# Kernel optimization log

Hardware: AMD Instinct MI355X
Metric: run time of the kernel (lower is better)

Reference implementation:

```python
import jax, jax.numpy as jnp
import numpy as np

EPS = 1e-6
NUM_HEADS = 16

def _rmsnorm(h, w):
    hf = h.astype(jnp.float32)
    var = jnp.mean(hf * hf, axis=-1, keepdims=True)
    return (w * (hf * jax.lax.rsqrt(var + EPS))).astype(h.dtype)

def _rotary(t, cos, sin):
    # t: [B,N,H,hd]; cos/sin: [N, hd//2]
    tf = t.astype(jnp.float32)
    tr = tf[..., 0::2]
    ti = tf[..., 1::2]
    c = cos[None, :, None, :]
    s = sin[None, :, None, :]
    out_r = tr * c - ti * s
    out_i = tr * s + ti * c
    out = jnp.stack([out_r, out_i], axis=-1).reshape(t.shape)
    return out.astype(t.dtype)

def setup_inputs() -> dict:
    key = jax.random.key(0)
    ks = jax.random.split(key, 8)
    B, N, C = 2, 2048, 1024
    hd = C // NUM_HEADS
    x = jax.random.normal(ks[0], (B, N, C), jnp.float32)
    qkv_w = jax.random.normal(ks[1], (3 * C, C), jnp.float32) * (C ** -0.5)
    q_norm_w = jnp.ones((hd,), jnp.float32)
    k_norm_w = jnp.ones((hd,), jnp.float32)
    proj_w = jax.random.normal(ks[2], (C, C), jnp.float32) * (C ** -0.5)
    proj_b = jnp.zeros((C,), jnp.float32)
    # rotary freqs_cis = exp(i * theta): unit-magnitude cos/sin
    inv_freq = 1.0 / (10000.0 ** (jnp.arange(0, hd, 2, dtype=jnp.float32) / hd))
    ang = jnp.arange(N, dtype=jnp.float32)[:, None] * inv_freq[None, :]
    pos_cos = jnp.cos(ang)
    pos_sin = jnp.sin(ang)
    mask = jnp.tril(jnp.ones((N, N), dtype=bool))
    return {"x": x, "qkv_w": qkv_w, "q_norm_w": q_norm_w, "k_norm_w": k_norm_w,
            "proj_w": proj_w, "proj_b": proj_b, "pos_cos": pos_cos,
            "pos_sin": pos_sin, "mask": mask}

def reference(x, qkv_w, q_norm_w, k_norm_w, proj_w, proj_b, pos_cos, pos_sin, mask):
    B, N, C = x.shape
    H = NUM_HEADS
    hd = C // H
    qkv = (x @ qkv_w.T).reshape(B, N, 3, H, hd)
    q, k, v = qkv[:, :, 0], qkv[:, :, 1], qkv[:, :, 2]  # [B,N,H,hd]
    q = _rmsnorm(q, q_norm_w)
    k = _rmsnorm(k, k_norm_w)
    q = _rotary(q, pos_cos, pos_sin)
    k = _rotary(k, pos_cos, pos_sin)
    q = q.transpose(0, 2, 1, 3)  # [B,H,N,hd]
    k = k.transpose(0, 2, 1, 3)
    v = v.transpose(0, 2, 1, 3)
    scale = hd ** -0.5
    scores = jnp.einsum('bhqd,bhkd->bhqk', q, k) * scale
    scores = jnp.where(mask[None, None, :, :], scores, jnp.float32(-1e30))
    attn = jax.nn.softmax(scores, axis=-1)
    out = jnp.einsum('bhqk,bhkd->bhqd', attn, v)
    out = out.transpose(0, 2, 1, 3).reshape(B, N, C)
    return out @ proj_w.T + proj_b
```

## Files before the change

### kernel.cpp

```cpp
#include <hip/hip_runtime.h>

using u16 = unsigned short;
using short4v = __attribute__((ext_vector_type(4))) short;
using short8 = __attribute__((ext_vector_type(8))) short;
using floatx4 = __attribute__((ext_vector_type(4))) float;

__device__ __forceinline__ float bf2f(u16 h) {
  union { unsigned int u; float f; } v;
  v.u = ((unsigned int)h) << 16;
  return v.f;
}
__device__ __forceinline__ u16 f2bf(float f) {
  union { float f; unsigned int u; } v;
  v.f = f;
  unsigned int u = v.u;
  return (u16)((u + 0x7FFFu + ((u >> 16) & 1u)) >> 16);
}
__device__ __forceinline__ u16 f2bf_rtz(float f) {
  union { float f; unsigned int u; } v;
  v.f = f;
  return (u16)(v.u >> 16);
}

typedef const __attribute__((address_space(1))) unsigned int* gas_t;
typedef __attribute__((address_space(3))) unsigned int* las_t;
__device__ __forceinline__ void gl_lds16(const u16* g, u16* l) {
  __builtin_amdgcn_global_load_lds((gas_t)(const void*)g, (las_t)(void*)l, 16,
                                   0, 0);
}

#define QSCALE 0.180336880111f

__global__ __launch_bounds__(256) void cvt_all(
    const float* __restrict__ x, const float* __restrict__ wq,
    const float* __restrict__ wp, u16* __restrict__ xb, u16* __restrict__ wqb,
    u16* __restrict__ wpb) {
  int i = blockIdx.x * 256 + threadIdx.x;
  const float* src;
  u16* dst;
  int off;
  if (i < 1048576) {
    src = x; dst = xb; off = i;
  } else if (i < 1048576 + 786432) {
    src = wq; dst = wqb; off = i - 1048576;
  } else {
    src = wp; dst = wpb; off = i - 1835008;
  }
  float4 v = ((const float4*)src)[off];
  ushort4 o;
  o.x = f2bf(v.x);
  o.y = f2bf(v.y);
  o.z = f2bf(v.z);
  o.w = f2bf(v.w);
  ((ushort4*)dst)[off] = o;
}

template <int BIAS, int OUTBF16, int MT>
__global__ __launch_bounds__(256) void gemm_nt(
    const u16* __restrict__ A, const u16* __restrict__ B,
    const float* __restrict__ bias, void* __restrict__ Cout,
    int M, int N, int K) {
  constexpr int ROWS_A = MT * 32;
  __shared__ u16 As[ROWS_A * 32];
  __shared__ u16 Bs[128 * 32];
  const int tid = threadIdx.x;
  const int lane = tid & 63;
  const int wave = tid >> 6;
  const int col = lane & 15;
  const int quad = lane >> 4;
  const int bm = blockIdx.y * ROWS_A;
  const int bn = blockIdx.x * 128;
  const int wm = (wave >> 1) * (MT * 16);
  const int wn = (wave & 1) * 64;

  floatx4 acc[MT][4] = {};

  for (int kb = 0; kb < K; kb += 32) {
    __syncthreads();
#pragma unroll
    for (int c = tid; c < ROWS_A * 4; c += 256)
      gl_lds16(A + (size_t)(bm + (c >> 2)) * K + kb + (c & 3) * 8, As + c * 8);
#pragma unroll
    for (int c = tid; c < 512; c += 256)
      gl_lds16(B + (size_t)(bn + (c >> 2)) * K + kb + (c & 3) * 8, Bs + c * 8);
    __syncthreads();

    short8 af[MT], bfr[4];
#pragma unroll
    for (int i = 0; i < MT; i++)
      af[i] = *(const short8*)(As + (wm + i * 16 + col) * 32 + quad * 8);
#pragma unroll
    for (int i = 0; i < 4; i++)
      bfr[i] = *(const short8*)(Bs + (wn + i * 16 + col) * 32 + quad * 8);
#pragma unroll
    for (int mi = 0; mi < MT; mi++)
#pragma unroll
      for (int ni = 0; ni < 4; ni++)
        acc[mi][ni] = __builtin_amdgcn_mfma_f32_16x16x32_bf16(
            af[mi], bfr[ni], acc[mi][ni], 0, 0, 0);
  }

#pragma unroll
  for (int mi = 0; mi < MT; mi++) {
#pragma unroll
    for (int ni = 0; ni < 4; ni++) {
#pragma unroll
      for (int r = 0; r < 4; r++) {
        int row = bm + wm + mi * 16 + quad * 4 + r;
        int c = bn + wn + ni * 16 + col;
        float v = acc[mi][ni][r];
        if (BIAS) v += bias[c];
        if (OUTBF16)
          ((u16*)Cout)[(size_t)row * N + c] = f2bf(v);
        else
          ((float*)Cout)[(size_t)row * N + c] = v;
      }
    }
  }
}

__global__ __launch_bounds__(256) void rope_v(
    const u16* __restrict__ qkv, const float* __restrict__ qw,
    const float* __restrict__ kw, const float* __restrict__ pcos,
    const float* __restrict__ psin, u16* __restrict__ Qb,
    u16* __restrict__ Kb, u16* __restrict__ Vt) {
  __shared__ u16 T[64 * 68];
  const int bh = blockIdx.x;
  const int n0 = blockIdx.y * 64;
  const int b = bh >> 4, h = bh & 15;
  const int tid = threadIdx.x;
  const int lane = tid & 63;
  const int wave = tid >> 6;

  const float qwl = qw[lane];
  const float kwl = kw[lane];
  for (int tt = 0; tt < 16; tt++) {
    const int n = n0 + wave * 16 + tt;
    const int t = b * 2048 + n;
    const u16* base = qkv + (size_t)t * 3072 + h * 64 + lane;
    float qv = bf2f(base[0]);
    float kv = bf2f(base[1024]);

    float sq = qv * qv, sk = kv * kv;
#pragma unroll
    for (int off = 32; off; off >>= 1) {
      sq += __shfl_xor(sq, off);
      sk += __shfl_xor(sk, off);
    }
    float qn = qv * rsqrtf(sq * (1.0f / 64.0f) + 1e-6f) * qwl;
    float kn = kv * rsqrtf(sk * (1.0f / 64.0f) + 1e-6f) * kwl;

    const int i = lane >> 1;
    const float c = pcos[n * 32 + i];
    const float s = psin[n * 32 + i];
    float qp = __shfl_xor(qn, 1);
    float kp = __shfl_xor(kn, 1);
    float qr, kr;
    if (lane & 1) {
      qr = qp * s + qn * c;
      kr = kp * s + kn * c;
    } else {
      qr = qn * c - qp * s;
      kr = kn * c - kp * s;
    }
    qr *= QSCALE;

    const size_t o = ((size_t)bh * 2048 + n) * 64 + lane;
    Qb[o] = f2bf(qr);
    Kb[o] = f2bf(kr);
  }

  const int q = tid & 7;
  const int r = tid >> 3;
#pragma unroll
  for (int rr = r; rr < 64; rr += 32) {
    short8 v = *(const short8*)(qkv + (size_t)(b * 2048 + n0 + rr) * 3072 +
                                2048 + h * 64 + q * 8);
    *(short8*)&T[rr * 68 + q * 8] = v;
  }
  __syncthreads();
#pragma unroll
  for (int dd = r; dd < 64; dd += 32) {
    short8 o;
#pragma unroll
    for (int j = 0; j < 8; j++) o[j] = T[(q * 8 + j) * 68 + dd];
    *(short8*)(Vt + (size_t)(bh * 64 + dd) * 2048 + n0 + q * 8) = o;
  }
}

#define PSTR 68
__global__ __launch_bounds__(256) void attn_flash(
    const u16* __restrict__ Q, const u16* __restrict__ Kk,
    const u16* __restrict__ Vt, u16* __restrict__ O) {
  __shared__ u16 Ks[2][2][64 * 32];
  __shared__ u16 Vs[2][2][64 * 32];
  __shared__ u16 Pb[4][16 * PSTR];
  const int id = blockIdx.x;
  const int bh = id & 31;
  const int tile = 31 - (id >> 5);
  const int tid = threadIdx.x;
  const int lane = tid & 63;
  const int wave = tid >> 6;
  const int col = lane & 15;
  const int quad = lane >> 4;
  const int srow = tid >> 2;
  const int sswz = ((tid & 3) ^ (srow & 3)) * 8;
  const int rq = (quad ^ (col & 3)) * 8;

  const u16* Qh = Q + (size_t)bh * 2048 * 64;
  const u16* Kh = Kk + (size_t)bh * 2048 * 64;
  const u16* Vh = Vt + (size_t)bh * 64 * 2048;
  const int b = bh >> 4, h = bh & 15;

  const int q0 = tile * 64 + wave * 16;

  short8 aq[2];
#pragma unroll
  for (int ks = 0; ks < 2; ks++)
    aq[ks] = *(const short8*)(Qh + (size_t)(q0 + col) * 64 + ks * 32 + quad * 8);

  short8 ones;
#pragma unroll
  for (int j = 0; j < 8; j++) ones[j] = (short)0x3F80;

  floatx4 accO[4] = {};
  floatx4 lacc = {};
  const int nsteps = tile + 1;

#pragma unroll
  for (int half = 0; half < 2; half++) {
    gl_lds16(Kh + (size_t)srow * 64 + half * 32 + sswz,
             &Ks[0][half][0] + tid * 8);
    gl_lds16(Vh + (size_t)srow * 2048 + half * 32 + sswz,
             &Vs[0][half][0] + tid * 8);
  }
  __syncthreads();

  int cur = 0;
  for (int kt = 0; kt < nsteps; kt++) {
    const int j0 = kt * 64;

    if (kt + 1 < nsteps) {
      const int j1 = j0 + 64;
#pragma unroll
      for (int half = 0; half < 2; half++) {
        gl_lds16(Kh + (size_t)(j1 + srow) * 64 + half * 32 + sswz,
                 &Ks[cur ^ 1][half][0] + tid * 8);
        gl_lds16(Vh + (size_t)srow * 2048 + j1 + half * 32 + sswz,
                 &Vs[cur ^ 1][half][0] + tid * 8);
      }
    }

    floatx4 s[4] = {};
#pragma unroll
    for (int nt = 0; nt < 4; nt++) {
#pragma unroll
      for (int ks = 0; ks < 2; ks++) {
        short8 bk = *(const short8*)&Ks[cur][ks][(nt * 16 + col) * 32 + rq];
        s[nt] =
            __builtin_amdgcn_mfma_f32_16x16x32_bf16(bk, aq[ks], s[nt], 0, 0, 0);
      }
    }

    if (j0 + 63 <= q0) {
#pragma unroll
      for (int nt = 0; nt < 4; nt++) {
        short4v pk;
#pragma unroll
        for (int r = 0; r < 4; r++)
          pk[r] = (short)f2bf_rtz(exp2f(s[nt][r]));
        *(short4v*)&Pb[wave][col * PSTR + nt * 16 + quad * 4] = pk;
      }
    } else {
      const int qg = q0 + col;
#pragma unroll
      for (int nt = 0; nt < 4; nt++) {
        const int jgb = j0 + nt * 16 + quad * 4;
        short4v pk;
#pragma unroll
        for (int r = 0; r < 4; r++) {
          float pv = (jgb + r <= qg) ? exp2f(s[nt][r]) : 0.0f;
          ll_unused:;
          pk[r] = (short)f2bf_rtz(pv);
        }
        *(short4v*)&Pb[wave][col * PSTR + nt * 16 + quad * 4] = pk;
      }
    }

    short8 ap[2];
#pragma unroll
    for (int kf = 0; kf < 2; kf++)
      ap[kf] = *(const short8*)&Pb[wave][col * PSTR + kf * 32 + quad * 8];

#pragma unroll
    for (int kf = 0; kf < 2; kf++)
      lacc = __builtin_amdgcn_mfma_f32_16x16x32_bf16(ap[kf], ones, lacc, 0, 0,
                                                     0);

#pragma unroll
    for (int nt = 0; nt < 4; nt++) {
#pragma unroll
      for (int kf = 0; kf < 2; kf++) {
        short8 bv = *(const short8*)&Vs[cur][kf][(nt * 16 + col) * 32 + rq];
        accO[nt] = __builtin_amdgcn_mfma_f32_16x16x32_bf16(ap[kf], bv,
                                                           accO[nt], 0, 0, 0);
      }
    }

    __syncthreads();
    cur ^= 1;
  }

  float lrec[4];
#pragma unroll
  for (int r = 0; r < 4; r++) lrec[r] = 1.0f / lacc[r];

#pragma unroll
  for (int nt = 0; nt < 4; nt++) {
#pragma unroll
    for (int r = 0; r < 4; r++) {
      int qg = q0 + quad * 4 + r;
      int d = nt * 16 + col;
      O[((size_t)(b * 2048 + qg) * 16 + h) * 64 + d] =
          f2bf(accO[nt][r] * lrec[r]);
    }
  }
}

extern "C" void kernel_launch(void* const* d_in, const int* in_sizes, int n_in,
                              void* d_out, int out_size, void* d_ws,
                              size_t ws_size, hipStream_t stream) {
  const float* x = (const float*)d_in[0];
  const float* qkv_w = (const float*)d_in[1];
  const float* q_norm_w = (const float*)d_in[2];
  const float* k_norm_w = (const float*)d_in[3];
  const float* proj_w = (const float*)d_in[4];
  const float* proj_b = (const float*)d_in[5];
  const float* pos_cos = (const float*)d_in[6];
  const float* pos_sin = (const float*)d_in[7];

  char* ws = (char*)d_ws;
  u16* xb = (u16*)ws;
  u16* wqkvb = (u16*)(ws + 8388608);
  u16* wprojb = (u16*)(ws + 14680064);
  u16* qkv = (u16*)(ws + 16777216);
  u16* Qb = (u16*)(ws + 41943040);
  u16* Kb = (u16*)(ws + 50331648);
  u16* Vt = (u16*)(ws + 58720256);
  u16* AO = (u16*)(ws + 67108864);

  cvt_all<<<8192, 256, 0, stream>>>(x, qkv_w, proj_w, xb, wqkvb, wprojb);

  gemm_nt<0, 1, 4><<<dim3(24, 32), 256, 0, stream>>>(xb, wqkvb, nullptr, qkv,
                                                     4096, 3072, 1024);

  rope_v<<<dim3(32, 32), 256, 0, stream>>>(qkv, q_norm_w, k_norm_w, pos_cos,
                                           pos_sin, Qb, Kb, Vt);

  attn_flash<<<dim3(1024), 256, 0, stream>>>(Qb, Kb, Vt, AO);

  gemm_nt<1, 0, 2><<<dim3(8, 64), 256, 0, stream>>>(AO, wprojb, proj_b,
                                                    (float*)d_out, 4096, 1024,
                                                    1024);
}
```

Baseline: 213.9 us.

## Pair long and short causal query tiles per attention block

```diff
diff --git a/kernel.cpp b/kernel.cpp
--- a/kernel.cpp
+++ b/kernel.cpp
@@ -197,7 +197,9 @@
   __shared__ u16 Pb[4][16 * PSTR];
   const int id = blockIdx.x;
   const int bh = id & 31;
-  const int tile = 31 - (id >> 5);
+  const int pair = id >> 5;
+  const int tileA = 31 - pair;
+  const int tileB = pair;
   const int tid = threadIdx.x;
   const int lane = tid & 63;
   const int wave = tid >> 6;
@@ -212,12 +214,19 @@
   const u16* Vh = Vt + (size_t)bh * 64 * 2048;
   const int b = bh >> 4, h = bh & 15;
 
-  const int q0 = tile * 64 + wave * 16;
-
-  short8 aq[2];
-#pragma unroll
-  for (int ks = 0; ks < 2; ks++)
-    aq[ks] = *(const short8*)(Qh + (size_t)(q0 + col) * 64 + ks * 32 + quad * 8);
+  const int q0A = tileA * 64 + wave * 16;
+  const int q0B = tileB * 64 + wave * 16;
+  const int nsA = tileA + 1;
+  const int nsB = tileB + 1;
+
+  short8 aqA[2], aqB[2];
+#pragma unroll
+  for (int ks = 0; ks < 2; ks++) {
+    aqA[ks] =
+        *(const short8*)(Qh + (size_t)(q0A + col) * 64 + ks * 32 + quad * 8);
+    aqB[ks] =
+        *(const short8*)(Qh + (size_t)(q0B + col) * 64 + ks * 32 + quad * 8);
+  }
 
   short8 ones;
 #pragma unroll
@@ -225,7 +234,97 @@
 
   floatx4 accO[4] = {};
   floatx4 lacc = {};
-  const int nsteps = tile + 1;
+  int cur = 0;
+
+  auto step = [&](int j0, int jnext, int q0, const short8* aq) {
+    if (jnext >= 0) {
+#pragma unroll
+      for (int half = 0; half < 2; half++) {
+        gl_lds16(Kh + (size_t)(jnext + srow) * 64 + half * 32 + sswz,
+                 &Ks[cur ^ 1][half][0] + tid * 8);
+        gl_lds16(Vh + (size_t)srow * 2048 + jnext + half * 32 + sswz,
+                 &Vs[cur ^ 1][half][0] + tid * 8);
+      }
+    }
+
+    floatx4 s[4] = {};
+#pragma unroll
+    for (int nt = 0; nt < 4; nt++) {
+#pragma unroll
+      for (int ks = 0; ks < 2; ks++) {
+        short8 bk = *(const short8*)&Ks[cur][ks][(nt * 16 + col) * 32 + rq];
+        s[nt] =
+            __builtin_amdgcn_mfma_f32_16x16x32_bf16(bk, aq[ks], s[nt], 0, 0, 0);
+      }
+    }
+
+    if (j0 + 63 <= q0) {
+#pragma unroll
+      for (int nt = 0; nt < 4; nt++) {
+        short4v pk;
+#pragma unroll
+        for (int r = 0; r < 4; r++)
+          pk[r] = (short)f2bf_rtz(exp2f(s[nt][r]));
+        *(short4v*)&Pb[wave][col * PSTR + nt * 16 + quad * 4] = pk;
+      }
+    } else {
+      const int qg = q0 + col;
+#pragma unroll
+      for (int nt = 0; nt < 4; nt++) {
+        const int jgb = j0 + nt * 16 + quad * 4;
+        short4v pk;
+#pragma unroll
+        for (int r = 0; r < 4; r++) {
+          float pv = (jgb + r <= qg) ? exp2f(s[nt][r]) : 0.0f;
+          pk[r] = (short)f2bf_rtz(pv);
+        }
+        *(short4v*)&Pb[wave][col * PSTR + nt * 16 + quad * 4] = pk;
+      }
+    }
+
+    short8 ap[2];
+#pragma unroll
+    for (int kf = 0; kf < 2; kf++)
+      ap[kf] = *(const short8*)&Pb[wave][col * PSTR + kf * 32 + quad * 8];
+
+#pragma unroll
+    for (int kf = 0; kf < 2; kf++)
+      lacc = __builtin_amdgcn_mfma_f32_16x16x32_bf16(ap[kf], ones, lacc, 0, 0,
+                                                     0);
+
+#pragma unroll
+    for (int nt = 0; nt < 4; nt++) {
+#pragma unroll
+      for (int kf = 0; kf < 2; kf++) {
+        short8 bv = *(const short8*)&Vs[cur][kf][(nt * 16 + col) * 32 + rq];
+        accO[nt] = __builtin_amdgcn_mfma_f32_16x16x32_bf16(ap[kf], bv,
+                                                           accO[nt], 0, 0, 0);
+      }
+    }
+
+    __syncthreads();
+    cur ^= 1;
+  };
+
+  auto finish = [&](int q0) {
+    float lrec[4];
+#pragma unroll
+    for (int r = 0; r < 4; r++) lrec[r] = 1.0f / lacc[r];
+#pragma unroll
+    for (int nt = 0; nt < 4; nt++) {
+#pragma unroll
+      for (int r = 0; r < 4; r++) {
+        int qg = q0 - wave * 16 + wave * 16 + quad * 4 + r;
+        int d = nt * 16 + col;
+        O[((size_t)(b * 2048 + (q0 + quad * 4 + r)) * 16 + h) * 64 + d] =
+            f2bf(accO[nt][r] * lrec[r]);
+        (void)qg;
+      }
+    }
+#pragma unroll
+    for (int nt = 0; nt < 4; nt++) accO[nt] = (floatx4){0.f, 0.f, 0.f, 0.f};
+    lacc = (floatx4){0.f, 0.f, 0.f, 0.f};
+  };
 
 #pragma unroll
   for (int half = 0; half < 2; half++) {
@@ -236,95 +335,13 @@
   }
   __syncthreads();
 
-  int cur = 0;
-  for (int kt = 0; kt < nsteps; kt++) {
-    const int j0 = kt * 64;
-
-    if (kt + 1 < nsteps) {
-      const int j1 = j0 + 64;
-#pragma unroll
-      for (int half = 0; half < 2; half++) {
-        gl_lds16(Kh + (size_t)(j1 + srow) * 64 + half * 32 + sswz,
-                 &Ks[cur ^ 1][half][0] + tid * 8);
-        gl_lds16(Vh + (size_t)srow * 2048 + j1 + half * 32 + sswz,
-                 &Vs[cur ^ 1][half][0] + tid * 8);
-      }
-    }
-
-    floatx4 s[4] = {};
-#pragma unroll
-    for (int nt = 0; nt < 4; nt++) {
-#pragma unroll
-      for (int ks = 0; ks < 2; ks++) {
-        short8 bk = *(const short8*)&Ks[cur][ks][(nt * 16 + col) * 32 + rq];
-        s[nt] =
-            __builtin_amdgcn_mfma_f32_16x16x32_bf16(bk, aq[ks], s[nt], 0, 0, 0);
-      }
-    }
-
-    if (j0 + 63 <= q0) {
-#pragma unroll
-      for (int nt = 0; nt < 4; nt++) {
-        short4v pk;
-#pragma unroll
-        for (int r = 0; r < 4; r++)
-          pk[r] = (short)f2bf_rtz(exp2f(s[nt][r]));
-        *(short4v*)&Pb[wave][col * PSTR + nt * 16 + quad * 4] = pk;
-      }
-    } else {
-      const int qg = q0 + col;
-#pragma unroll
-      for (int nt = 0; nt < 4; nt++) {
-        const int jgb = j0 + nt * 16 + quad * 4;
-        short4v pk;
-#pragma unroll
-        for (int r = 0; r < 4; r++) {
-          float pv = (jgb + r <= qg) ? exp2f(s[nt][r]) : 0.0f;
-          ll_unused:;
-          pk[r] = (short)f2bf_rtz(pv);
-        }
-        *(short4v*)&Pb[wave][col * PSTR + nt * 16 + quad * 4] = pk;
-      }
-    }
-
-    short8 ap[2];
-#pragma unroll
-    for (int kf = 0; kf < 2; kf++)
-      ap[kf] = *(const short8*)&Pb[wave][col * PSTR + kf * 32 + quad * 8];
-
-#pragma unroll
-    for (int kf = 0; kf < 2; kf++)
-      lacc = __builtin_amdgcn_mfma_f32_16x16x32_bf16(ap[kf], ones, lacc, 0, 0,
-                                                     0);
-
-#pragma unroll
-    for (int nt = 0; nt < 4; nt++) {
-#pragma unroll
-      for (int kf = 0; kf < 2; kf++) {
-        short8 bv = *(const short8*)&Vs[cur][kf][(nt * 16 + col) * 32 + rq];
-        accO[nt] = __builtin_amdgcn_mfma_f32_16x16x32_bf16(ap[kf], bv,
-                                                           accO[nt], 0, 0, 0);
-      }
-    }
-
-    __syncthreads();
-    cur ^= 1;
-  }
-
-  float lrec[4];
-#pragma unroll
-  for (int r = 0; r < 4; r++) lrec[r] = 1.0f / lacc[r];
-
-#pragma unroll
-  for (int nt = 0; nt < 4; nt++) {
-#pragma unroll
-    for (int r = 0; r < 4; r++) {
-      int qg = q0 + quad * 4 + r;
-      int d = nt * 16 + col;
-      O[((size_t)(b * 2048 + qg) * 16 + h) * 64 + d] =
-          f2bf(accO[nt][r] * lrec[r]);
-    }
-  }
+  for (int kt = 0; kt < nsA; kt++)
+    step(kt * 64, (kt + 1 < nsA) ? (kt + 1) * 64 : 0, q0A, aqA);
+  finish(q0A);
+
+  for (int kt = 0; kt < nsB; kt++)
+    step(kt * 64, (kt + 1 < nsB) ? (kt + 1) * 64 : -1, q0B, aqB);
+  finish(q0B);
 }
 
 extern "C" void kernel_launch(void* const* d_in, const int* in_sizes, int n_in,
@@ -357,7 +374,7 @@
   rope_v<<<dim3(32, 32), 256, 0, stream>>>(qkv, q_norm_w, k_norm_w, pos_cos,
                                            pos_sin, Qb, Kb, Vt);
 
-  attn_flash<<<dim3(1024), 256, 0, stream>>>(Qb, Kb, Vt, AO);
+  attn_flash<<<dim3(512), 256, 0, stream>>>(Qb, Kb, Vt, AO);
 
   gemm_nt<1, 0, 2><<<dim3(8, 64), 256, 0, stream>>>(AO, wprojb, proj_b,
                                                     (float*)d_out, 4096, 1024,
```

Result: no change. 211.4 us (-1.2%).

## Double GEMM K-tile to 64 with XOR-swizzled LDS layout

Applied to the files above, without the earlier changes.

```diff
diff --git a/kernel.cpp b/kernel.cpp
--- a/kernel.cpp
+++ b/kernel.cpp
@@ -28,6 +28,8 @@
   __builtin_amdgcn_global_load_lds((gas_t)(const void*)g, (las_t)(void*)l, 16,
                                    0, 0);
 }
+
+#define MFMA32 __builtin_amdgcn_mfma_f32_16x16x32_bf16
 
 #define QSCALE 0.180336880111f
 
@@ -61,8 +63,8 @@
     const float* __restrict__ bias, void* __restrict__ Cout,
     int M, int N, int K) {
   constexpr int ROWS_A = MT * 32;
-  __shared__ u16 As[ROWS_A * 32];
-  __shared__ u16 Bs[128 * 32];
+  __shared__ u16 As[ROWS_A * 64];
+  __shared__ u16 Bs[128 * 64];
   const int tid = threadIdx.x;
   const int lane = tid & 63;
   const int wave = tid >> 6;
@@ -72,32 +74,41 @@
   const int bn = blockIdx.x * 128;
   const int wm = (wave >> 1) * (MT * 16);
   const int wn = (wave & 1) * 64;
+  const int rsw = col & 7;
 
   floatx4 acc[MT][4] = {};
 
-  for (int kb = 0; kb < K; kb += 32) {
+  for (int kb = 0; kb < K; kb += 64) {
     __syncthreads();
 #pragma unroll
-    for (int c = tid; c < ROWS_A * 4; c += 256)
-      gl_lds16(A + (size_t)(bm + (c >> 2)) * K + kb + (c & 3) * 8, As + c * 8);
-#pragma unroll
-    for (int c = tid; c < 512; c += 256)
-      gl_lds16(B + (size_t)(bn + (c >> 2)) * K + kb + (c & 3) * 8, Bs + c * 8);
+    for (int c = tid; c < ROWS_A * 8; c += 256) {
+      const int row = c >> 3, s = (c & 7) ^ (row & 7);
+      gl_lds16(A + (size_t)(bm + row) * K + kb + s * 8, As + c * 8);
+    }
+#pragma unroll
+    for (int c = tid; c < 1024; c += 256) {
+      const int row = c >> 3, s = (c & 7) ^ (row & 7);
+      gl_lds16(B + (size_t)(bn + row) * K + kb + s * 8, Bs + c * 8);
+    }
     __syncthreads();
 
-    short8 af[MT], bfr[4];
-#pragma unroll
-    for (int i = 0; i < MT; i++)
-      af[i] = *(const short8*)(As + (wm + i * 16 + col) * 32 + quad * 8);
-#pragma unroll
-    for (int i = 0; i < 4; i++)
-      bfr[i] = *(const short8*)(Bs + (wn + i * 16 + col) * 32 + quad * 8);
-#pragma unroll
-    for (int mi = 0; mi < MT; mi++)
-#pragma unroll
-      for (int ni = 0; ni < 4; ni++)
-        acc[mi][ni] = __builtin_amdgcn_mfma_f32_16x16x32_bf16(
-            af[mi], bfr[ni], acc[mi][ni], 0, 0, 0);
+#pragma unroll
+    for (int kk = 0; kk < 2; kk++) {
+      short8 af[MT], bfr[4];
+#pragma unroll
+      for (int i = 0; i < MT; i++)
+        af[i] = *(const short8*)(As + (wm + i * 16 + col) * 64 +
+                                 ((kk * 4 + quad) ^ rsw) * 8);
+#pragma unroll
+      for (int i = 0; i < 4; i++)
+        bfr[i] = *(const short8*)(Bs + (wn + i * 16 + col) * 64 +
+                                  ((kk * 4 + quad) ^ rsw) * 8);
+#pragma unroll
+      for (int mi = 0; mi < MT; mi++)
+#pragma unroll
+        for (int ni = 0; ni < 4; ni++)
+          acc[mi][ni] = MFMA32(af[mi], bfr[ni], acc[mi][ni], 0, 0, 0);
+    }
   }
 
 #pragma unroll
@@ -257,8 +268,7 @@
 #pragma unroll
       for (int ks = 0; ks < 2; ks++) {
         short8 bk = *(const short8*)&Ks[cur][ks][(nt * 16 + col) * 32 + rq];
-        s[nt] =
-            __builtin_amdgcn_mfma_f32_16x16x32_bf16(bk, aq[ks], s[nt], 0, 0, 0);
+        s[nt] = MFMA32(bk, aq[ks], s[nt], 0, 0, 0);
       }
     }
 
@@ -280,7 +290,6 @@
 #pragma unroll
         for (int r = 0; r < 4; r++) {
           float pv = (jgb + r <= qg) ? exp2f(s[nt][r]) : 0.0f;
-          ll_unused:;
           pk[r] = (short)f2bf_rtz(pv);
         }
         *(short4v*)&Pb[wave][col * PSTR + nt * 16 + quad * 4] = pk;
@@ -294,16 +303,14 @@
 
 #pragma unroll
     for (int kf = 0; kf < 2; kf++)
-      lacc = __builtin_amdgcn_mfma_f32_16x16x32_bf16(ap[kf], ones, lacc, 0, 0,
-                                                     0);
+      lacc = MFMA32(ap[kf], ones, lacc, 0, 0, 0);
 
 #pragma unroll
     for (int nt = 0; nt < 4; nt++) {
 #pragma unroll
       for (int kf = 0; kf < 2; kf++) {
         short8 bv = *(const short8*)&Vs[cur][kf][(nt * 16 + col) * 32 + rq];
-        accO[nt] = __builtin_amdgcn_mfma_f32_16x16x32_bf16(ap[kf], bv,
-                                                           accO[nt], 0, 0, 0);
+        accO[nt] = MFMA32(ap[kf], bv, accO[nt], 0, 0, 0);
       }
     }
 
```

New measurement: 208.3 us. 1.03x faster.
